# Performance work log

Measured on AMD Instinct MI355X. Metric: run time of the kernel, lower is better.

## Reference

```python
import jax, jax.numpy as jnp
import numpy as np

N = 100000   # total input points
NP = 50000   # output (pooled) points N'
K = 32       # neighbors per output point
F = 128      # feature dim


def setup_inputs() -> dict:
    key = jax.random.key(0)
    k1, k2, k3 = jax.random.split(key, 3)
    points = jax.random.normal(k1, (N, 3), dtype=jnp.float32)
    features = jax.random.normal(k2, (N, F), dtype=jnp.float32)
    neighbor_indices = jax.random.randint(k3, (NP, K), 0, N, dtype=jnp.int64)
    return {"points": points, "features": features, "neighbor_indices": neighbor_indices}


def reference(points, features, neighbor_indices):
    # gather neighbor features: (N', K, F), then max-pool over neighbor axis
    neighbor_features = features[neighbor_indices]  # (N', K, F)
    return jnp.max(neighbor_features, axis=1)       # (N', F)
```

## Files before the change

### kernel.cpp

```cpp
#include <hip/hip_runtime.h>
#include <math.h>


__global__ __launch_bounds__(256) void pool_max_sorted(
    const float4* __restrict__ feat4,
    const int*    __restrict__ nbr,
    float4*       __restrict__ out4,
    int NP)
{
    __shared__ alignas(16) int lds_idx[32 * 32];

    const int t = threadIdx.x;

    {
        size_t gbase = (size_t)blockIdx.x * 1024 + (size_t)t * 4;
        int4 v = make_int4(0, 0, 0, 0);
        if (gbase < (size_t)NP * 32)
            v = *(const int4*)(nbr + gbase);
        *(int4*)&lds_idx[t * 4] = v;
    }
    __syncthreads();

    {
        const int lane31 = t & 31;
        const int s = t >> 5;
        for (int r = 0; r < 4; ++r) {
            const int pl = s + r * 8;
            int v = lds_idx[pl * 32 + lane31];
            #pragma unroll
            for (int k = 2; k <= 32; k <<= 1) {
                #pragma unroll
                for (int j = k >> 1; j > 0; j >>= 1) {
                    int o = __shfl_xor(v, j, 32);
                    bool lower = (lane31 & j) == 0;
                    bool up    = (lane31 & k) == 0;
                    int mn = v < o ? v : o;
                    int mx = v < o ? o : v;
                    v = (lower == up) ? mn : mx;
                }
            }
            lds_idx[pl * 32 + lane31] = v;
        }
    }
    __syncthreads();

    const int g = t >> 3;
    const int l = t & 7;
    const int p = blockIdx.x * 32 + g;
    if (p >= NP) return;

    const int4* sj = (const int4*)&lds_idx[g * 32];
    float4 m0 = make_float4(-INFINITY, -INFINITY, -INFINITY, -INFINITY);
    float4 m1 = m0, m2 = m0, m3 = m0;

    #pragma unroll
    for (int kb = 0; kb < 8; ++kb) {
        int4 jj = sj[kb];
        {
            const float4* b = feat4 + (size_t)jj.x * 32 + l;
            float4 v0 = b[0], v1 = b[8], v2 = b[16], v3 = b[24];
            m0.x = fmaxf(m0.x, v0.x); m0.y = fmaxf(m0.y, v0.y); m0.z = fmaxf(m0.z, v0.z); m0.w = fmaxf(m0.w, v0.w);
            m1.x = fmaxf(m1.x, v1.x); m1.y = fmaxf(m1.y, v1.y); m1.z = fmaxf(m1.z, v1.z); m1.w = fmaxf(m1.w, v1.w);
            m2.x = fmaxf(m2.x, v2.x); m2.y = fmaxf(m2.y, v2.y); m2.z = fmaxf(m2.z, v2.z); m2.w = fmaxf(m2.w, v2.w);
            m3.x = fmaxf(m3.x, v3.x); m3.y = fmaxf(m3.y, v3.y); m3.z = fmaxf(m3.z, v3.z); m3.w = fmaxf(m3.w, v3.w);
        }
        {
            const float4* b = feat4 + (size_t)jj.y * 32 + l;
            float4 v0 = b[0], v1 = b[8], v2 = b[16], v3 = b[24];
            m0.x = fmaxf(m0.x, v0.x); m0.y = fmaxf(m0.y, v0.y); m0.z = fmaxf(m0.z, v0.z); m0.w = fmaxf(m0.w, v0.w);
            m1.x = fmaxf(m1.x, v1.x); m1.y = fmaxf(m1.y, v1.y); m1.z = fmaxf(m1.z, v1.z); m1.w = fmaxf(m1.w, v1.w);
            m2.x = fmaxf(m2.x, v2.x); m2.y = fmaxf(m2.y, v2.y); m2.z = fmaxf(m2.z, v2.z); m2.w = fmaxf(m2.w, v2.w);
            m3.x = fmaxf(m3.x, v3.x); m3.y = fmaxf(m3.y, v3.y); m3.z = fmaxf(m3.z, v3.z); m3.w = fmaxf(m3.w, v3.w);
        }
        {
            const float4* b = feat4 + (size_t)jj.z * 32 + l;
            float4 v0 = b[0], v1 = b[8], v2 = b[16], v3 = b[24];
            m0.x = fmaxf(m0.x, v0.x); m0.y = fmaxf(m0.y, v0.y); m0.z = fmaxf(m0.z, v0.z); m0.w = fmaxf(m0.w, v0.w);
            m1.x = fmaxf(m1.x, v1.x); m1.y = fmaxf(m1.y, v1.y); m1.z = fmaxf(m1.z, v1.z); m1.w = fmaxf(m1.w, v1.w);
            m2.x = fmaxf(m2.x, v2.x); m2.y = fmaxf(m2.y, v2.y); m2.z = fmaxf(m2.z, v2.z); m2.w = fmaxf(m2.w, v2.w);
            m3.x = fmaxf(m3.x, v3.x); m3.y = fmaxf(m3.y, v3.y); m3.z = fmaxf(m3.z, v3.z); m3.w = fmaxf(m3.w, v3.w);
        }
        {
            const float4* b = feat4 + (size_t)jj.w * 32 + l;
            float4 v0 = b[0], v1 = b[8], v2 = b[16], v3 = b[24];
            m0.x = fmaxf(m0.x, v0.x); m0.y = fmaxf(m0.y, v0.y); m0.z = fmaxf(m0.z, v0.z); m0.w = fmaxf(m0.w, v0.w);
            m1.x = fmaxf(m1.x, v1.x); m1.y = fmaxf(m1.y, v1.y); m1.z = fmaxf(m1.z, v1.z); m1.w = fmaxf(m1.w, v1.w);
            m2.x = fmaxf(m2.x, v2.x); m2.y = fmaxf(m2.y, v2.y); m2.z = fmaxf(m2.z, v2.z); m2.w = fmaxf(m2.w, v2.w);
            m3.x = fmaxf(m3.x, v3.x); m3.y = fmaxf(m3.y, v3.y); m3.z = fmaxf(m3.z, v3.z); m3.w = fmaxf(m3.w, v3.w);
        }
    }

    float4* ob = out4 + (size_t)p * 32 + l;
    ob[0]  = m0;
    ob[8]  = m1;
    ob[16] = m2;
    ob[24] = m3;
}

extern "C" void kernel_launch(void* const* d_in, const int* in_sizes, int n_in,
                              void* d_out, int out_size, void* d_ws, size_t ws_size,
                              hipStream_t stream) {
    const float* features = (const float*)d_in[1];
    const int*   nbr      = (const int*)d_in[2];
    float*       out      = (float*)d_out;

    const int F = 128;
    int NP = out_size / F;

    const int threads = 256;
    int grid = (NP + 31) / 32;
    pool_max_sorted<<<grid, threads, 0, stream>>>(
        (const float4*)features, nbr, (float4*)out, NP);
}
```

Before: 187.8 us.

## Pace neighbor gathers through row-range phases with block barriers

Replaces the fully unrolled 32-neighbor gather with a loop over 16 row-range phases. In each phase a point group consumes its sorted indices below the phase threshold, two rows at a time, and the block synchronizes between phases. The intent is to keep concurrent accesses within a narrow band of feature rows to improve cache locality. In exchange it adds data-dependent loops, divergence, barriers, and fewer outstanding loads per thread.

```diff
diff --git a/kernel.cpp b/kernel.cpp
--- a/kernel.cpp
+++ b/kernel.cpp
@@ -2,14 +2,13 @@
 #include <math.h>
 
 
-__global__ __launch_bounds__(256) void pool_max_sorted(
+__global__ __launch_bounds__(256) void pool_max_paced(
     const float4* __restrict__ feat4,
     const int*    __restrict__ nbr,
     float4*       __restrict__ out4,
-    int NP)
+    int NP, int Nrows)
 {
     __shared__ alignas(16) int lds_idx[32 * 32];
-
     const int t = threadIdx.x;
 
     {
@@ -47,54 +46,55 @@
     const int g = t >> 3;
     const int l = t & 7;
     const int p = blockIdx.x * 32 + g;
-    if (p >= NP) return;
+    const bool active = (p < NP);
+    const int* sj = &lds_idx[g * 32];
 
-    const int4* sj = (const int4*)&lds_idx[g * 32];
     float4 m0 = make_float4(-INFINITY, -INFINITY, -INFINITY, -INFINITY);
     float4 m1 = m0, m2 = m0, m3 = m0;
+    int ptr = 0;
 
-    #pragma unroll
-    for (int kb = 0; kb < 8; ++kb) {
-        int4 jj = sj[kb];
-        {
-            const float4* b = feat4 + (size_t)jj.x * 32 + l;
-            float4 v0 = b[0], v1 = b[8], v2 = b[16], v3 = b[24];
-            m0.x = fmaxf(m0.x, v0.x); m0.y = fmaxf(m0.y, v0.y); m0.z = fmaxf(m0.z, v0.z); m0.w = fmaxf(m0.w, v0.w);
-            m1.x = fmaxf(m1.x, v1.x); m1.y = fmaxf(m1.y, v1.y); m1.z = fmaxf(m1.z, v1.z); m1.w = fmaxf(m1.w, v1.w);
-            m2.x = fmaxf(m2.x, v2.x); m2.y = fmaxf(m2.y, v2.y); m2.z = fmaxf(m2.z, v2.z); m2.w = fmaxf(m2.w, v2.w);
-            m3.x = fmaxf(m3.x, v3.x); m3.y = fmaxf(m3.y, v3.y); m3.z = fmaxf(m3.z, v3.z); m3.w = fmaxf(m3.w, v3.w);
+    #pragma unroll 1
+    for (int s = 0; s < 16; ++s) {
+        int thresh = (int)(((long long)(s + 1) * (long long)Nrows) >> 4);
+        if (active) {
+            while (ptr < 32 && sj[ptr] < thresh) {
+                int j0 = sj[ptr];
+                bool two = (ptr + 1 < 32) && (sj[ptr + 1] < thresh);
+                int j1 = two ? sj[ptr + 1] : j0;
+                ptr += two ? 2 : 1;
+
+                const float4* a = feat4 + (size_t)j0 * 32 + l;
+                const float4* b = feat4 + (size_t)j1 * 32 + l;
+                float4 a0 = a[0], a1 = a[8], a2 = a[16], a3 = a[24];
+                float4 b0 = b[0], b1 = b[8], b2 = b[16], b3 = b[24];
+                m0.x = fmaxf(m0.x, fmaxf(a0.x, b0.x));
+                m0.y = fmaxf(m0.y, fmaxf(a0.y, b0.y));
+                m0.z = fmaxf(m0.z, fmaxf(a0.z, b0.z));
+                m0.w = fmaxf(m0.w, fmaxf(a0.w, b0.w));
+                m1.x = fmaxf(m1.x, fmaxf(a1.x, b1.x));
+                m1.y = fmaxf(m1.y, fmaxf(a1.y, b1.y));
+                m1.z = fmaxf(m1.z, fmaxf(a1.z, b1.z));
+                m1.w = fmaxf(m1.w, fmaxf(a1.w, b1.w));
+                m2.x = fmaxf(m2.x, fmaxf(a2.x, b2.x));
+                m2.y = fmaxf(m2.y, fmaxf(a2.y, b2.y));
+                m2.z = fmaxf(m2.z, fmaxf(a2.z, b2.z));
+                m2.w = fmaxf(m2.w, fmaxf(a2.w, b2.w));
+                m3.x = fmaxf(m3.x, fmaxf(a3.x, b3.x));
+                m3.y = fmaxf(m3.y, fmaxf(a3.y, b3.y));
+                m3.z = fmaxf(m3.z, fmaxf(a3.z, b3.z));
+                m3.w = fmaxf(m3.w, fmaxf(a3.w, b3.w));
+            }
         }
-        {
-            const float4* b = feat4 + (size_t)jj.y * 32 + l;
-            float4 v0 = b[0], v1 = b[8], v2 = b[16], v3 = b[24];
-            m0.x = fmaxf(m0.x, v0.x); m0.y = fmaxf(m0.y, v0.y); m0.z = fmaxf(m0.z, v0.z); m0.w = fmaxf(m0.w, v0.w);
-            m1.x = fmaxf(m1.x, v1.x); m1.y = fmaxf(m1.y, v1.y); m1.z = fmaxf(m1.z, v1.z); m1.w = fmaxf(m1.w, v1.w);
-            m2.x = fmaxf(m2.x, v2.x); m2.y = fmaxf(m2.y, v2.y); m2.z = fmaxf(m2.z, v2.z); m2.w = fmaxf(m2.w, v2.w);
-            m3.x = fmaxf(m3.x, v3.x); m3.y = fmaxf(m3.y, v3.y); m3.z = fmaxf(m3.z, v3.z); m3.w = fmaxf(m3.w, v3.w);
-        }
-        {
-            const float4* b = feat4 + (size_t)jj.z * 32 + l;
-            float4 v0 = b[0], v1 = b[8], v2 = b[16], v3 = b[24];
-            m0.x = fmaxf(m0.x, v0.x); m0.y = fmaxf(m0.y, v0.y); m0.z = fmaxf(m0.z, v0.z); m0.w = fmaxf(m0.w, v0.w);
-            m1.x = fmaxf(m1.x, v1.x); m1.y = fmaxf(m1.y, v1.y); m1.z = fmaxf(m1.z, v1.z); m1.w = fmaxf(m1.w, v1.w);
-            m2.x = fmaxf(m2.x, v2.x); m2.y = fmaxf(m2.y, v2.y); m2.z = fmaxf(m2.z, v2.z); m2.w = fmaxf(m2.w, v2.w);
-            m3.x = fmaxf(m3.x, v3.x); m3.y = fmaxf(m3.y, v3.y); m3.z = fmaxf(m3.z, v3.z); m3.w = fmaxf(m3.w, v3.w);
-        }
-        {
-            const float4* b = feat4 + (size_t)jj.w * 32 + l;
-            float4 v0 = b[0], v1 = b[8], v2 = b[16], v3 = b[24];
-            m0.x = fmaxf(m0.x, v0.x); m0.y = fmaxf(m0.y, v0.y); m0.z = fmaxf(m0.z, v0.z); m0.w = fmaxf(m0.w, v0.w);
-            m1.x = fmaxf(m1.x, v1.x); m1.y = fmaxf(m1.y, v1.y); m1.z = fmaxf(m1.z, v1.z); m1.w = fmaxf(m1.w, v1.w);
-            m2.x = fmaxf(m2.x, v2.x); m2.y = fmaxf(m2.y, v2.y); m2.z = fmaxf(m2.z, v2.z); m2.w = fmaxf(m2.w, v2.w);
-            m3.x = fmaxf(m3.x, v3.x); m3.y = fmaxf(m3.y, v3.y); m3.z = fmaxf(m3.z, v3.z); m3.w = fmaxf(m3.w, v3.w);
-        }
+        __syncthreads();
     }
 
-    float4* ob = out4 + (size_t)p * 32 + l;
-    ob[0]  = m0;
-    ob[8]  = m1;
-    ob[16] = m2;
-    ob[24] = m3;
+    if (active) {
+        float4* ob = out4 + (size_t)p * 32 + l;
+        ob[0]  = m0;
+        ob[8]  = m1;
+        ob[16] = m2;
+        ob[24] = m3;
+    }
 }
 
 extern "C" void kernel_launch(void* const* d_in, const int* in_sizes, int n_in,
@@ -105,10 +105,11 @@
     float*       out      = (float*)d_out;
 
     const int F = 128;
-    int NP = out_size / F;
+    int NP    = out_size / F;
+    int Nrows = in_sizes[1] / F;
 
     const int threads = 256;
     int grid = (NP + 31) / 32;
-    pool_max_sorted<<<grid, threads, 0, stream>>>(
-        (const float4*)features, nbr, (float4*)out, NP);
+    pool_max_paced<<<grid, threads, 0, stream>>>(
+        (const float4*)features, nbr, (float4*)out, NP, Nrows);
 }
```

After: 186.6 us. Within noise of the previous version (-0.6%).
